# Kernel tuning notes

Measured on AMD Instinct MI355X. Metric: run time of the kernel, lower is better.

## Reference

```python
import jax, jax.numpy as jnp
import numpy as np

V, D, H = 5000, 300, 256
B, T = 16, 512


def setup_inputs() -> dict:
    key = jax.random.key(0)
    ks = jax.random.split(key, 14)
    def w(k, shape):
        return jax.random.normal(k, shape, dtype=jnp.float32) * 0.02
    return {
        "x": jax.random.normal(ks[0], (B, T, V), dtype=jnp.float32),
        "hidden_state": jax.random.normal(ks[1], (1, H), dtype=jnp.float32),
        "context_state": jax.random.normal(ks[2], (1, H), dtype=jnp.float32),
        "E": w(ks[3], (D, V)),      # embedding Linear weight [out,in]
        "Wf": w(ks[4], (H, D)), "Uf": w(ks[5], (H, H)),
        "Wg": w(ks[6], (H, D)), "Ug": w(ks[7], (H, H)),
        "Wi": w(ks[8], (H, D)), "Ui": w(ks[9], (H, H)),
        "Wo": w(ks[10], (H, D)), "Uo": w(ks[11], (H, H)),
        "Wout": w(ks[12], (V, H)),
    }


def reference(x, hidden_state, context_state, E, Wf, Uf, Wg, Ug, Wi, Ui, Wo, Uo, Wout):
    # Precompute all input-side projections in one batched pass: [B,T,D]
    emb = jnp.einsum('btv,dv->btd', x, E)
    # Stack input-gate GEMMs: [B,T,4H]
    Wx = jnp.concatenate([Wf, Wg, Wi, Wo], axis=0)  # [4H, D]
    gates_x = jnp.einsum('btd,gd->btg', emb, Wx)    # [B, T, 4H]
    Uh = jnp.concatenate([Uf, Ug, Ui, Uo], axis=0)  # [4H, H]

    h0 = jnp.broadcast_to(hidden_state, (x.shape[0], hidden_state.shape[-1]))
    c0 = jnp.broadcast_to(context_state, (x.shape[0], context_state.shape[-1]))

    Hn = hidden_state.shape[-1]

    def step(carry, gx):
        h, c = carry
        gh = h @ Uh.T                     # [B, 4H]
        z = gx + gh
        f = jax.nn.sigmoid(z[:, 0*Hn:1*Hn])
        g = jnp.tanh(z[:, 1*Hn:2*Hn])
        i = jax.nn.sigmoid(z[:, 2*Hn:3*Hn])
        o = jax.nn.sigmoid(z[:, 3*Hn:4*Hn])
        c_new = g * i + c * f
        h_new = o * jnp.tanh(c_new)
        # NOTE: faithful to source - output projects g, not h
        out = g @ Wout.T                  # [B, V]
        return (h_new, c_new), out

    _, outs = jax.lax.scan(step, (h0, c0), jnp.swapaxes(gates_x, 0, 1))
    return jnp.swapaxes(outs, 0, 1)       # [B, T, V]
```

## Files before the change

### kernel.cpp

```cpp
#include <hip/hip_runtime.h>
#include <stdint.h>

typedef unsigned short u16;
typedef unsigned int u32;
typedef __attribute__((ext_vector_type(8))) __bf16 bf16x8;
typedef __attribute__((ext_vector_type(4))) float f32x4;
typedef __attribute__((ext_vector_type(4))) u32 u32x4;
typedef __attribute__((ext_vector_type(2))) u32 u32x2;
typedef __attribute__((ext_vector_type(4))) int i32x4;

#define DEV __device__ __forceinline__

constexpr int V = 5000, D = 300, H = 256, BB = 16, T = 512;
constexpr int M = BB * T;
constexpr int DP = 320;
constexpr int KP = 5024;
constexpr int G4 = 1024;
constexpr int NPAD = 5120;

constexpr size_t OFF_EB    = 0;
constexpr size_t OFF_WXB   = OFF_EB    + (size_t)DP * KP * 2;
constexpr size_t OFF_UHB   = OFF_WXB   + (size_t)G4 * DP * 2;
constexpr size_t OFF_WOUTB = OFF_UHB   + (size_t)G4 * H * 2;
constexpr size_t OFF_GATES = OFF_WOUTB + (size_t)NPAD * H * 2;
constexpr size_t OFF_GALL  = OFF_GATES + (size_t)T * BB * G4 * 2;
constexpr size_t OFF_EMB   = OFF_GALL  + (size_t)M * H * 2;

DEV u16 f2bf(float f) {
  u32 i = __builtin_bit_cast(u32, f);
  return (u16)((i + 0x7FFFu + ((i >> 16) & 1u)) >> 16);
}
DEV float bf2f(u16 u) { return __builtin_bit_cast(float, (u32)u << 16); }
DEV f32x4 MFMA(u32x4 a, u32x4 b, f32x4 c) {
  return __builtin_amdgcn_mfma_f32_16x16x32_bf16(
      __builtin_bit_cast(bf16x8, a), __builtin_bit_cast(bf16x8, b), c, 0, 0, 0);
}
DEV i32x4 MFMA8(u32x4 a, u32x4 b, i32x4 c) {
  return __builtin_amdgcn_mfma_i32_16x16x64_i8(
      __builtin_bit_cast(i32x4, a), __builtin_bit_cast(i32x4, b), c, 0, 0, 0);
}
DEV float sigm(float x) { return 1.f / (1.f + __expf(-x)); }
DEV float tanh_s(float x) { float e = __expf(2.f * x); return 1.f - 2.f / (e + 1.f); }

DEV void bar_lds() {
  asm volatile("s_waitcnt lgkmcnt(0)" ::: "memory");
  __builtin_amdgcn_sched_barrier(0);
  __builtin_amdgcn_s_barrier();
  __builtin_amdgcn_sched_barrier(0);
}

__global__ __launch_bounds__(256) void k_prep(
    const float* __restrict__ E, const float* __restrict__ Wf, const float* __restrict__ Wg,
    const float* __restrict__ Wi, const float* __restrict__ Wo,
    const float* __restrict__ Wout, char* __restrict__ ws) {
  u16* Eb = (u16*)(ws + OFF_EB);
  u16* Wxb = (u16*)(ws + OFF_WXB);
  u16* Wob = (u16*)(ws + OFF_WOUTB);

  const int NE = DP * KP, NW = G4 * DP, NWO = NPAD * H;
  const int total = NE + NW + NWO;
  for (int i = blockIdx.x * blockDim.x + threadIdx.x; i < total; i += gridDim.x * blockDim.x) {
    int j = i;
    if (j < NE) {
      int nn = j / KP, k = j % KP;
      Eb[j] = f2bf((nn < D && k < V) ? E[(size_t)nn * V + k] : 0.f);
      continue;
    }
    j -= NE;
    if (j < NW) {
      int r = j / DP, k = j % DP;
      const float* Wp = (r < 256) ? Wf : (r < 512) ? Wg : (r < 768) ? Wi : Wo;
      Wxb[j] = f2bf((k < D) ? Wp[(size_t)(r & 255) * D + k] : 0.f);
      continue;
    }
    j -= NW;
    if (j < NWO) {
      int nn = j / H, k = j % H;
      Wob[j] = f2bf((nn < V) ? Wout[(size_t)nn * H + k] : 0.f);
      continue;
    }
  }
}

__global__ __launch_bounds__(256) void k_prep_u(
    const float* __restrict__ Uf, const float* __restrict__ Ug,
    const float* __restrict__ Ui, const float* __restrict__ Uo, char* __restrict__ ws) {
  char* qU = ws + OFF_UHB;
  float* zsc = (float*)(ws + OFF_UHB + (size_t)G4 * H);
  const int row = blockIdx.x * 4 + (threadIdx.x >> 6);
  const int lane = threadIdx.x & 63;
  const float* Up = (row < 256) ? Uf : (row < 512) ? Ug : (row < 768) ? Ui : Uo;
  f32x4 v = *(const f32x4*)(Up + (size_t)(row & 255) * H + lane * 4);
  float m = fmaxf(fmaxf(fabsf(v[0]), fabsf(v[1])), fmaxf(fabsf(v[2]), fabsf(v[3])));
  for (int i = 1; i < 64; i <<= 1) m = fmaxf(m, __shfl_xor(m, i));
  float inv = (m > 0.f) ? 127.f / m : 0.f;
  int q0 = (int)rintf(v[0] * inv), q1 = (int)rintf(v[1] * inv);
  int q2 = (int)rintf(v[2] * inv), q3 = (int)rintf(v[3] * inv);
  q0 = max(-127, min(127, q0)); q1 = max(-127, min(127, q1));
  q2 = max(-127, min(127, q2)); q3 = max(-127, min(127, q3));
  u32 pk = (u32)(q0 & 255) | ((u32)(q1 & 255) << 8) | ((u32)(q2 & 255) << 16) |
           ((u32)(q3 & 255) << 24);
  *(u32*)(qU + (size_t)row * H + lane * 4) = pk;
  if (lane == 0) zsc[row] = m / 16129.f;
}

__global__ __launch_bounds__(256) void k_emb(const float* __restrict__ x, char* __restrict__ ws) {
  const u16* Eb = (const u16*)(ws + OFF_EB);
  float* emb = (float*)(ws + OFF_EMB);
  __shared__ __align__(16) u16 As[32 * 40];
  __shared__ __align__(16) u16 Bs[320 * 40];

  const int tid = threadIdx.x;
  const int m0 = blockIdx.x * 32;
  const int lane = tid & 63, wv = tid >> 6;
  const int l15 = lane & 15, lc = lane >> 4;
  const int mt = wv & 1, ntb = (wv >> 1) * 10;

  f32x4 acc[10];
#pragma unroll
  for (int j = 0; j < 10; j++) acc[j] = (f32x4){0.f, 0.f, 0.f, 0.f};

  const int ar = tid >> 3, ak = (tid & 7) * 4;

  f32x4 xv0, xv1;
  u32x4 ev0[5], ev1[5];

#define EMB_ISSUE(SFX, KS)                                                        \
  do {                                                                            \
    int k0_ = (KS) * 32;                                                          \
    {                                                                             \
      size_t base_ = (size_t)(m0 + ar) * V + k0_ + ak;                            \
      if (k0_ + ak + 3 < V) {                                                     \
        xv##SFX = *(const f32x4*)(x + base_);                                     \
      } else {                                                                    \
        f32x4 t_;                                                                 \
        t_[0] = (k0_ + ak + 0 < V) ? x[base_ + 0] : 0.f;                          \
        t_[1] = (k0_ + ak + 1 < V) ? x[base_ + 1] : 0.f;                          \
        t_[2] = (k0_ + ak + 2 < V) ? x[base_ + 2] : 0.f;                          \
        t_[3] = (k0_ + ak + 3 < V) ? x[base_ + 3] : 0.f;                          \
        xv##SFX = t_;                                                             \
      }                                                                           \
    }                                                                             \
    _Pragma("unroll") for (int j_ = 0; j_ < 5; j_++) {                            \
      int cc_ = tid + 256 * j_;                                                   \
      int n_ = cc_ >> 2, ko_ = (cc_ & 3) * 8;                                     \
      ev##SFX[j_] = *(const u32x4*)(Eb + (size_t)n_ * KP + k0_ + ko_);            \
    }                                                                             \
  } while (0)

#define EMB_WRITE(SFX)                                                            \
  do {                                                                            \
    union { u16 u[4]; u32x2 v; } ua_;                                             \
    ua_.u[0] = f2bf(xv##SFX[0]); ua_.u[1] = f2bf(xv##SFX[1]);                     \
    ua_.u[2] = f2bf(xv##SFX[2]); ua_.u[3] = f2bf(xv##SFX[3]);                     \
    *(u32x2*)&As[ar * 40 + ak] = ua_.v;                                           \
    _Pragma("unroll") for (int j_ = 0; j_ < 5; j_++) {                            \
      int cc_ = tid + 256 * j_;                                                   \
      int n_ = cc_ >> 2, ko_ = (cc_ & 3) * 8;                                     \
      *(u32x4*)&Bs[n_ * 40 + ko_] = ev##SFX[j_];                                  \
    }                                                                             \
  } while (0)

  auto emb_compute = [&]() {
    u32x4 a = *(const u32x4*)&As[(mt * 16 + l15) * 40 + lc * 8];
#pragma unroll
    for (int j = 0; j < 10; j++) {
      u32x4 b = *(const u32x4*)&Bs[((ntb + j) * 16 + l15) * 40 + lc * 8];
      acc[j] = MFMA(a, b, acc[j]);
    }
  };

  constexpr int NK = 157;
  EMB_ISSUE(0, 0);
  EMB_ISSUE(1, 1);
  for (int ks = 0; ks < NK; ks += 2) {
    __syncthreads();
    EMB_WRITE(0);
    if (ks + 2 < NK) EMB_ISSUE(0, ks + 2);
    __syncthreads();
    emb_compute();
    if (ks + 1 < NK) {
      __syncthreads();
      EMB_WRITE(1);
      if (ks + 3 < NK) EMB_ISSUE(1, ks + 3);
      __syncthreads();
      emb_compute();
    }
  }
#pragma unroll
  for (int j = 0; j < 10; j++) {
    int nn = (ntb + j) * 16 + l15;
    int mrow = m0 + mt * 16 + lc * 4;
#pragma unroll
    for (int r = 0; r < 4; r++) emb[(size_t)(mrow + r) * DP + nn] = acc[j][r];
  }
#undef EMB_ISSUE
#undef EMB_WRITE
}

__global__ __launch_bounds__(256) void k_gates(char* __restrict__ ws) {
  const float* emb = (const float*)(ws + OFF_EMB);
  const u16* Wxb = (const u16*)(ws + OFF_WXB);
  u16* gates = (u16*)(ws + OFF_GATES);
  __shared__ __align__(16) u16 As[64 * 40];
  __shared__ __align__(16) u16 Bs[256 * 40];

  const int tid = threadIdx.x;
  const int blk = blockIdx.x;
  const int m0 = (blk >> 2) * 64, n0 = (blk & 3) * 256;
  const int lane = tid & 63, wv = tid >> 6;
  const int l15 = lane & 15, lc = lane >> 4;

  f32x4 acc[16];
#pragma unroll
  for (int j = 0; j < 16; j++) acc[j] = (f32x4){0.f, 0.f, 0.f, 0.f};

  f32x4 av0[2], av1[2];
  u32x4 bv0[4], bv1[4];

#define GT_ISSUE(SFX, KS)                                                         \
  do {                                                                            \
    int k0_ = (KS) * 32;                                                          \
    _Pragma("unroll") for (int j_ = 0; j_ < 2; j_++) {                            \
      int c_ = tid + 256 * j_;                                                    \
      int r_ = c_ >> 3, ko_ = (c_ & 7) * 4;                                       \
      av##SFX[j_] = *(const f32x4*)(emb + (size_t)(m0 + r_) * DP + k0_ + ko_);    \
    }                                                                             \
    _Pragma("unroll") for (int j_ = 0; j_ < 4; j_++) {                            \
      int c_ = tid + 256 * j_;                                                    \
      int n_ = c_ >> 2, ko_ = (c_ & 3) * 8;                                       \
      bv##SFX[j_] = *(const u32x4*)(Wxb + (size_t)(n0 + n_) * DP + k0_ + ko_);    \
    }                                                                             \
  } while (0)

#define GT_WRITE(SFX)                                                             \
  do {                                                                            \
    _Pragma("unroll") for (int j_ = 0; j_ < 2; j_++) {                            \
      int c_ = tid + 256 * j_;                                                    \
      int r_ = c_ >> 3, ko_ = (c_ & 7) * 4;                                       \
      union { u16 u[4]; u32x2 v; } ua_;                                           \
      ua_.u[0] = f2bf(av##SFX[j_][0]); ua_.u[1] = f2bf(av##SFX[j_][1]);           \
      ua_.u[2] = f2bf(av##SFX[j_][2]); ua_.u[3] = f2bf(av##SFX[j_][3]);           \
      *(u32x2*)&As[r_ * 40 + ko_] = ua_.v;                                        \
    }                                                                             \
    _Pragma("unroll") for (int j_ = 0; j_ < 4; j_++) {                            \
      int c_ = tid + 256 * j_;                                                    \
      int n_ = c_ >> 2, ko_ = (c_ & 3) * 8;                                       \
      *(u32x4*)&Bs[n_ * 40 + ko_] = bv##SFX[j_];                                  \
    }                                                                             \
  } while (0)

  auto gt_compute = [&]() {
    u32x4 a = *(const u32x4*)&As[(wv * 16 + l15) * 40 + lc * 8];
#pragma unroll
    for (int nt = 0; nt < 16; nt++) {
      u32x4 b = *(const u32x4*)&Bs[(nt * 16 + l15) * 40 + lc * 8];
      acc[nt] = MFMA(a, b, acc[nt]);
    }
  };

  constexpr int NK = 10;
  GT_ISSUE(0, 0);
  GT_ISSUE(1, 1);
  for (int ks = 0; ks < NK; ks += 2) {
    __syncthreads();
    GT_WRITE(0);
    if (ks + 2 < NK) GT_ISSUE(0, ks + 2);
    __syncthreads();
    gt_compute();
    __syncthreads();
    GT_WRITE(1);
    if (ks + 3 < NK) GT_ISSUE(1, ks + 3);
    __syncthreads();
    gt_compute();
  }
#pragma unroll
  for (int nt = 0; nt < 16; nt++) {
#pragma unroll
    for (int r = 0; r < 4; r++) {
      int m = m0 + wv * 16 + lc * 4 + r;
      int col = n0 + nt * 16 + l15;
      int q = col >> 8, nn = col & 255;
      gates[(((size_t)(m & (T - 1)) * 16 + (m >> 9)) * 256 + nn) * 4 + q] = f2bf(acc[nt][r]);
    }
  }
#undef GT_ISSUE
#undef GT_WRITE
}

__global__ __launch_bounds__(512) void k_scan(const float* __restrict__ hidden,
                                              const float* __restrict__ ctx,
                                              char* __restrict__ ws) {
  const char* qU = (const char*)(ws + OFF_UHB);
  const float* zsc = (const float*)(ws + OFF_UHB + (size_t)G4 * H);
  const u16* gates = (const u16*)(ws + OFF_GATES);
  u16* gall = (u16*)(ws + OFF_GALL);

  __shared__ __align__(16) char pq[2][2][256];
  __shared__ __align__(16) int zw[2][8][8][2][16];

  const int tid = threadIdx.x;
  const int lane = tid & 63, wv = tid >> 6;
  const int l15 = lane & 15, lc = lane >> 4;

  u32x4 uq[4][2][4];
#pragma unroll
  for (int gg = 0; gg < 4; gg++)
#pragma unroll
    for (int j = 0; j < 2; j++)
#pragma unroll
      for (int kt = 0; kt < 4; kt++)
        uq[gg][j][kt] = *(const u32x4*)(
            qU + (size_t)(gg * 256 + wv * 32 + j * 16 + l15) * H + kt * 64 + lc * 16);

  const int b = lane >> 5, np = lane & 31;
  const int n = wv * 32 + np;
  const int jj = (np >> 4) & 1, rr = np & 15;
  const int b_glob = blockIdx.x * 2 + b;
  float c = ctx[n];
  const float zs0 = zsc[n], zs1 = zsc[n + 256], zs2 = zsc[n + 512], zs3 = zsc[n + 768];
  u32x2 gxc = *(const u32x2*)(gates + (((size_t)0 * 16 + b_glob) * 256 + n) * 4);
  u32x2 gxn = *(const u32x2*)(gates + (((size_t)1 * 16 + b_glob) * 256 + n) * 4);

  {
    const int b0 = tid >> 8, n0i = tid & 255;
    float h0 = hidden[n0i];
    h0 = fminf(3.999f, fmaxf(-3.999f, h0));
    pq[0][b0][n0i] = (char)(int)rintf(h0 * 31.75f);
  }
  __syncthreads();

#pragma unroll 1
  for (int t = 0; t < T; ++t) {
    const int par = t & 1;
    u32x4 bfr[4];
#pragma unroll
    for (int kt = 0; kt < 4; kt++)
      bfr[kt] = *(const u32x4*)&pq[par][l15 & 1][kt * 64 + lc * 16];

    i32x4 acc[4][2];
#pragma unroll
    for (int gg = 0; gg < 4; gg++)
#pragma unroll
      for (int j = 0; j < 2; j++) {
        i32x4 a = {0, 0, 0, 0};
#pragma unroll
        for (int kt = 0; kt < 4; kt++) a = MFMA8(uq[gg][j][kt], bfr[kt], a);
        acc[gg][j] = a;
      }
    if (l15 < 2) {
#pragma unroll
      for (int gg = 0; gg < 4; gg++)
#pragma unroll
        for (int j = 0; j < 2; j++)
          *(i32x4*)&zw[par][wv][gg * 2 + j][l15][lc * 4] = acc[gg][j];
    }
    asm volatile("s_waitcnt lgkmcnt(0)" ::: "memory");
    __builtin_amdgcn_sched_barrier(0);

    const float hs = (t == 0) ? 4.f : 1.f;
    float z0 = (float)zw[par][wv][0 + jj][b][rr] * (zs0 * hs) + bf2f((u16)(gxc[0] & 0xFFFFu));
    float z1 = (float)zw[par][wv][2 + jj][b][rr] * (zs1 * hs) + bf2f((u16)(gxc[0] >> 16));
    float z2 = (float)zw[par][wv][4 + jj][b][rr] * (zs2 * hs) + bf2f((u16)(gxc[1] & 0xFFFFu));
    float z3 = (float)zw[par][wv][6 + jj][b][rr] * (zs3 * hs) + bf2f((u16)(gxc[1] >> 16));
    float fv = sigm(z0), gv = tanh_s(z1), iv = sigm(z2), ov = sigm(z3);
    c = gv * iv + c * fv;
    float hn = ov * tanh_s(c);
    gall[((size_t)b_glob * T + t) * H + n] = f2bf(gv);
    pq[par ^ 1][b][n] = (char)(int)rintf(hn * 127.f);
    gxc = gxn;
    int t2 = (t + 2 < T) ? (t + 2) : t;
    gxn = *(const u32x2*)(gates + (((size_t)t2 * 16 + b_glob) * 256 + n) * 4);
    bar_lds();
  }
}

__global__ __launch_bounds__(256) void k_out(char* __restrict__ ws, float* __restrict__ out) {
  const u16* gall = (const u16*)(ws + OFF_GALL);
  const u16* Wob = (const u16*)(ws + OFF_WOUTB);
  __shared__ __align__(16) u16 As[64 * 40];
  __shared__ __align__(16) u16 Bs[256 * 40];

  const int tid = threadIdx.x;
  const int blk = blockIdx.x;
  const int m0 = (blk / 20) * 64, n0 = (blk % 20) * 256;
  const int lane = tid & 63, wv = tid >> 6;
  const int l15 = lane & 15, lc = lane >> 4;

  f32x4 acc[16];
#pragma unroll
  for (int j = 0; j < 16; j++) acc[j] = (f32x4){0.f, 0.f, 0.f, 0.f};

  u32x4 av0, av1;
  u32x4 bv0[4], bv1[4];

#define OUT_ISSUE(SFX, KS)                                                        \
  do {                                                                            \
    int k0_ = (KS) * 32;                                                          \
    {                                                                             \
      int r_ = tid >> 2, ko_ = (tid & 3) * 8;                                     \
      av##SFX = *(const u32x4*)(gall + (size_t)(m0 + r_) * H + k0_ + ko_);        \
    }                                                                             \
    _Pragma("unroll") for (int j_ = 0; j_ < 4; j_++) {                            \
      int c_ = tid + 256 * j_;                                                    \
      int n_ = c_ >> 2, ko_ = (c_ & 3) * 8;                                       \
      bv##SFX[j_] = *(const u32x4*)(Wob + (size_t)(n0 + n_) * H + k0_ + ko_);     \
    }                                                                             \
  } while (0)

#define OUT_WRITE(SFX)                                                            \
  do {                                                                            \
    {                                                                             \
      int r_ = tid >> 2, ko_ = (tid & 3) * 8;                                     \
      *(u32x4*)&As[r_ * 40 + ko_] = av##SFX;                                      \
    }                                                                             \
    _Pragma("unroll") for (int j_ = 0; j_ < 4; j_++) {                            \
      int c_ = tid + 256 * j_;                                                    \
      int n_ = c_ >> 2, ko_ = (c_ & 3) * 8;                                       \
      *(u32x4*)&Bs[n_ * 40 + ko_] = bv##SFX[j_];                                  \
    }                                                                             \
  } while (0)

  auto out_compute = [&]() {
    u32x4 a = *(const u32x4*)&As[(wv * 16 + l15) * 40 + lc * 8];
#pragma unroll
    for (int nt = 0; nt < 16; nt++) {
      u32x4 b = *(const u32x4*)&Bs[(nt * 16 + l15) * 40 + lc * 8];
      acc[nt] = MFMA(a, b, acc[nt]);
    }
  };

  constexpr int NK = 8;
  OUT_ISSUE(0, 0);
  OUT_ISSUE(1, 1);
  for (int ks = 0; ks < NK; ks += 2) {
    __syncthreads();
    OUT_WRITE(0);
    if (ks + 2 < NK) OUT_ISSUE(0, ks + 2);
    __syncthreads();
    out_compute();
    __syncthreads();
    OUT_WRITE(1);
    if (ks + 3 < NK) OUT_ISSUE(1, ks + 3);
    __syncthreads();
    out_compute();
  }
#pragma unroll
  for (int nt = 0; nt < 16; nt++) {
    int vcol = n0 + nt * 16 + l15;
    if (vcol < V) {
#pragma unroll
      for (int r = 0; r < 4; r++) {
        int m = m0 + wv * 16 + lc * 4 + r;
        out[(size_t)m * V + vcol] = acc[nt][r];
      }
    }
  }
#undef OUT_ISSUE
#undef OUT_WRITE
}

extern "C" void kernel_launch(void* const* d_in, const int* in_sizes, int n_in,
                              void* d_out, int out_size, void* d_ws, size_t ws_size,
                              hipStream_t stream) {
  (void)in_sizes; (void)n_in; (void)out_size; (void)ws_size;
  const float* x      = (const float*)d_in[0];
  const float* hidden = (const float*)d_in[1];
  const float* ctx    = (const float*)d_in[2];
  const float* E      = (const float*)d_in[3];
  const float* Wf     = (const float*)d_in[4];
  const float* Uf     = (const float*)d_in[5];
  const float* Wg     = (const float*)d_in[6];
  const float* Ug     = (const float*)d_in[7];
  const float* Wi     = (const float*)d_in[8];
  const float* Ui     = (const float*)d_in[9];
  const float* Wo     = (const float*)d_in[10];
  const float* Uo     = (const float*)d_in[11];
  const float* Wout   = (const float*)d_in[12];
  char* ws = (char*)d_ws;
  float* out = (float*)d_out;

  hipLaunchKernelGGL(k_prep, dim3(1024), dim3(256), 0, stream,
                     E, Wf, Wg, Wi, Wo, Wout, ws);
  hipLaunchKernelGGL(k_prep_u, dim3(256), dim3(256), 0, stream, Uf, Ug, Ui, Uo, ws);
  hipLaunchKernelGGL(k_emb, dim3(M / 32), dim3(256), 0, stream, x, ws);
  hipLaunchKernelGGL(k_gates, dim3((M / 64) * 4), dim3(256), 0, stream, ws);
  hipLaunchKernelGGL(k_scan, dim3(8), dim3(512), 0, stream, hidden, ctx, ws);
  hipLaunchKernelGGL(k_out, dim3((M / 64) * 20), dim3(256), 0, stream, ws, out);
}
```

Measured before the change: 822.8 us.

## Fuse embedding and gate GEMMs, merge prep kernels, vectorize output stores

Merges the U-quantization prep into the main prep kernel and fuses the embedding GEMM with the gate projection GEMM, keeping the bf16 embedding tile in LDS instead of round-tripping fp32 emb through global memory. The fused kernel uses 512-thread blocks over 256 tiles of 32 rows, reading Wx directly from global in the second stage. The output GEMM now stages accumulators through LDS to emit coalesced 16-byte stores. Risks include lower parallelism (only 256 blocks for the large x-reading GEMM), uncached global reads of Wx, and the tail column guard dropping the last partial vector if V is not a multiple of 4.

```diff
diff --git a/kernel.cpp b/kernel.cpp
--- a/kernel.cpp
+++ b/kernel.cpp
@@ -24,7 +24,6 @@
 constexpr size_t OFF_WOUTB = OFF_UHB   + (size_t)G4 * H * 2;
 constexpr size_t OFF_GATES = OFF_WOUTB + (size_t)NPAD * H * 2;
 constexpr size_t OFF_GALL  = OFF_GATES + (size_t)T * BB * G4 * 2;
-constexpr size_t OFF_EMB   = OFF_GALL  + (size_t)M * H * 2;
 
 DEV u16 f2bf(float f) {
   u32 i = __builtin_bit_cast(u32, f);
@@ -52,14 +51,35 @@
 __global__ __launch_bounds__(256) void k_prep(
     const float* __restrict__ E, const float* __restrict__ Wf, const float* __restrict__ Wg,
     const float* __restrict__ Wi, const float* __restrict__ Wo,
+    const float* __restrict__ Uf, const float* __restrict__ Ug,
+    const float* __restrict__ Ui, const float* __restrict__ Uo,
     const float* __restrict__ Wout, char* __restrict__ ws) {
+  if (blockIdx.x >= 1024) {
+    char* qU = ws + OFF_UHB;
+    float* zsc = (float*)(ws + OFF_UHB + (size_t)G4 * H);
+    const int row = (blockIdx.x - 1024) * 4 + (threadIdx.x >> 6);
+    const int lane = threadIdx.x & 63;
+    const float* Up = (row < 256) ? Uf : (row < 512) ? Ug : (row < 768) ? Ui : Uo;
+    f32x4 v = *(const f32x4*)(Up + (size_t)(row & 255) * H + lane * 4);
+    float m = fmaxf(fmaxf(fabsf(v[0]), fabsf(v[1])), fmaxf(fabsf(v[2]), fabsf(v[3])));
+    for (int i = 1; i < 64; i <<= 1) m = fmaxf(m, __shfl_xor(m, i));
+    float inv = (m > 0.f) ? 127.f / m : 0.f;
+    int q0 = (int)rintf(v[0] * inv), q1 = (int)rintf(v[1] * inv);
+    int q2 = (int)rintf(v[2] * inv), q3 = (int)rintf(v[3] * inv);
+    q0 = max(-127, min(127, q0)); q1 = max(-127, min(127, q1));
+    q2 = max(-127, min(127, q2)); q3 = max(-127, min(127, q3));
+    u32 pk = (u32)(q0 & 255) | ((u32)(q1 & 255) << 8) | ((u32)(q2 & 255) << 16) |
+             ((u32)(q3 & 255) << 24);
+    *(u32*)(qU + (size_t)row * H + lane * 4) = pk;
+    if (lane == 0) zsc[row] = m / 16129.f;
+    return;
+  }
   u16* Eb = (u16*)(ws + OFF_EB);
   u16* Wxb = (u16*)(ws + OFF_WXB);
   u16* Wob = (u16*)(ws + OFF_WOUTB);
-
   const int NE = DP * KP, NW = G4 * DP, NWO = NPAD * H;
   const int total = NE + NW + NWO;
-  for (int i = blockIdx.x * blockDim.x + threadIdx.x; i < total; i += gridDim.x * blockDim.x) {
+  for (int i = blockIdx.x * blockDim.x + threadIdx.x; i < total; i += 1024 * blockDim.x) {
     int j = i;
     if (j < NE) {
       int nn = j / KP, k = j % KP;
@@ -82,54 +102,34 @@
   }
 }
 
-__global__ __launch_bounds__(256) void k_prep_u(
-    const float* __restrict__ Uf, const float* __restrict__ Ug,
-    const float* __restrict__ Ui, const float* __restrict__ Uo, char* __restrict__ ws) {
-  char* qU = ws + OFF_UHB;
-  float* zsc = (float*)(ws + OFF_UHB + (size_t)G4 * H);
-  const int row = blockIdx.x * 4 + (threadIdx.x >> 6);
-  const int lane = threadIdx.x & 63;
-  const float* Up = (row < 256) ? Uf : (row < 512) ? Ug : (row < 768) ? Ui : Uo;
-  f32x4 v = *(const f32x4*)(Up + (size_t)(row & 255) * H + lane * 4);
-  float m = fmaxf(fmaxf(fabsf(v[0]), fabsf(v[1])), fmaxf(fabsf(v[2]), fabsf(v[3])));
-  for (int i = 1; i < 64; i <<= 1) m = fmaxf(m, __shfl_xor(m, i));
-  float inv = (m > 0.f) ? 127.f / m : 0.f;
-  int q0 = (int)rintf(v[0] * inv), q1 = (int)rintf(v[1] * inv);
-  int q2 = (int)rintf(v[2] * inv), q3 = (int)rintf(v[3] * inv);
-  q0 = max(-127, min(127, q0)); q1 = max(-127, min(127, q1));
-  q2 = max(-127, min(127, q2)); q3 = max(-127, min(127, q3));
-  u32 pk = (u32)(q0 & 255) | ((u32)(q1 & 255) << 8) | ((u32)(q2 & 255) << 16) |
-           ((u32)(q3 & 255) << 24);
-  *(u32*)(qU + (size_t)row * H + lane * 4) = pk;
-  if (lane == 0) zsc[row] = m / 16129.f;
-}
-
-__global__ __launch_bounds__(256) void k_emb(const float* __restrict__ x, char* __restrict__ ws) {
-  const u16* Eb = (const u16*)(ws + OFF_EB);
-  float* emb = (float*)(ws + OFF_EMB);
+__global__ __launch_bounds__(512) void k_embgates(const float* __restrict__ x,
+                                                  char* __restrict__ ws) {
   __shared__ __align__(16) u16 As[32 * 40];
   __shared__ __align__(16) u16 Bs[320 * 40];
+  __shared__ __align__(16) u16 embS[32 * 328];
+  const u16* Eb = (const u16*)(ws + OFF_EB);
+  const u16* Wxb = (const u16*)(ws + OFF_WXB);
+  u16* gates = (u16*)(ws + OFF_GATES);
 
   const int tid = threadIdx.x;
-  const int m0 = blockIdx.x * 32;
   const int lane = tid & 63, wv = tid >> 6;
   const int l15 = lane & 15, lc = lane >> 4;
-  const int mt = wv & 1, ntb = (wv >> 1) * 10;
-
-  f32x4 acc[10];
-#pragma unroll
-  for (int j = 0; j < 10; j++) acc[j] = (f32x4){0.f, 0.f, 0.f, 0.f};
-
+  const int it = blockIdx.x;
+  const int tc = it >> 4, b = it & 15;
+  const int m0x = b * T + tc * 32;
+
+  f32x4 acc[5];
+#pragma unroll
+  for (int j = 0; j < 5; j++) acc[j] = (f32x4){0.f, 0.f, 0.f, 0.f};
   const int ar = tid >> 3, ak = (tid & 7) * 4;
-
   f32x4 xv0, xv1;
-  u32x4 ev0[5], ev1[5];
-
-#define EMB_ISSUE(SFX, KS)                                                        \
+  u32x4 ev0[3], ev1[3];
+
+#define WEMB_ISSUE(SFX, KS)                                                       \
   do {                                                                            \
     int k0_ = (KS) * 32;                                                          \
-    {                                                                             \
-      size_t base_ = (size_t)(m0 + ar) * V + k0_ + ak;                            \
+    if (tid < 256) {                                                              \
+      size_t base_ = (size_t)(m0x + ar) * V + k0_ + ak;                           \
       if (k0_ + ak + 3 < V) {                                                     \
         xv##SFX = *(const f32x4*)(x + base_);                                     \
       } else {                                                                    \
@@ -141,151 +141,95 @@
         xv##SFX = t_;                                                             \
       }                                                                           \
     }                                                                             \
-    _Pragma("unroll") for (int j_ = 0; j_ < 5; j_++) {                            \
-      int cc_ = tid + 256 * j_;                                                   \
-      int n_ = cc_ >> 2, ko_ = (cc_ & 3) * 8;                                     \
-      ev##SFX[j_] = *(const u32x4*)(Eb + (size_t)n_ * KP + k0_ + ko_);            \
+    _Pragma("unroll") for (int p_ = 0; p_ < 3; p_++) {                            \
+      int cc_ = tid + 512 * p_;                                                   \
+      if (cc_ < 1280) {                                                           \
+        int n_ = cc_ >> 2, ko_ = (cc_ & 3) * 8;                                   \
+        ev##SFX[p_] = *(const u32x4*)(Eb + (size_t)n_ * KP + k0_ + ko_);          \
+      }                                                                           \
     }                                                                             \
   } while (0)
 
-#define EMB_WRITE(SFX)                                                            \
+#define WEMB_WRITE(SFX)                                                           \
   do {                                                                            \
-    union { u16 u[4]; u32x2 v; } ua_;                                             \
-    ua_.u[0] = f2bf(xv##SFX[0]); ua_.u[1] = f2bf(xv##SFX[1]);                     \
-    ua_.u[2] = f2bf(xv##SFX[2]); ua_.u[3] = f2bf(xv##SFX[3]);                     \
-    *(u32x2*)&As[ar * 40 + ak] = ua_.v;                                           \
-    _Pragma("unroll") for (int j_ = 0; j_ < 5; j_++) {                            \
-      int cc_ = tid + 256 * j_;                                                   \
-      int n_ = cc_ >> 2, ko_ = (cc_ & 3) * 8;                                     \
-      *(u32x4*)&Bs[n_ * 40 + ko_] = ev##SFX[j_];                                  \
+    if (tid < 256) {                                                              \
+      union { u16 u[4]; u32x2 v; } ua_;                                           \
+      ua_.u[0] = f2bf(xv##SFX[0]); ua_.u[1] = f2bf(xv##SFX[1]);                   \
+      ua_.u[2] = f2bf(xv##SFX[2]); ua_.u[3] = f2bf(xv##SFX[3]);                   \
+      *(u32x2*)&As[ar * 40 + ak] = ua_.v;                                         \
+    }                                                                             \
+    _Pragma("unroll") for (int p_ = 0; p_ < 3; p_++) {                            \
+      int cc_ = tid + 512 * p_;                                                   \
+      if (cc_ < 1280) {                                                           \
+        int n_ = cc_ >> 2, ko_ = (cc_ & 3) * 8;                                   \
+        *(u32x4*)&Bs[n_ * 40 + ko_] = ev##SFX[p_];                                \
+      }                                                                           \
     }                                                                             \
   } while (0)
 
-  auto emb_compute = [&]() {
+  const int mt = wv & 1, ntb = (wv >> 1) * 5;
+  auto wemb_compute = [&]() {
     u32x4 a = *(const u32x4*)&As[(mt * 16 + l15) * 40 + lc * 8];
 #pragma unroll
-    for (int j = 0; j < 10; j++) {
-      u32x4 b = *(const u32x4*)&Bs[((ntb + j) * 16 + l15) * 40 + lc * 8];
-      acc[j] = MFMA(a, b, acc[j]);
+    for (int j = 0; j < 5; j++) {
+      u32x4 bb = *(const u32x4*)&Bs[((ntb + j) * 16 + l15) * 40 + lc * 8];
+      acc[j] = MFMA(a, bb, acc[j]);
     }
   };
 
   constexpr int NK = 157;
-  EMB_ISSUE(0, 0);
-  EMB_ISSUE(1, 1);
+  WEMB_ISSUE(0, 0);
+  WEMB_ISSUE(1, 1);
   for (int ks = 0; ks < NK; ks += 2) {
     __syncthreads();
-    EMB_WRITE(0);
-    if (ks + 2 < NK) EMB_ISSUE(0, ks + 2);
-    __syncthreads();
-    emb_compute();
+    WEMB_WRITE(0);
+    if (ks + 2 < NK) WEMB_ISSUE(0, ks + 2);
+    __syncthreads();
+    wemb_compute();
     if (ks + 1 < NK) {
       __syncthreads();
-      EMB_WRITE(1);
-      if (ks + 3 < NK) EMB_ISSUE(1, ks + 3);
+      WEMB_WRITE(1);
+      if (ks + 3 < NK) WEMB_ISSUE(1, ks + 3);
       __syncthreads();
-      emb_compute();
-    }
-  }
-#pragma unroll
-  for (int j = 0; j < 10; j++) {
+      wemb_compute();
+    }
+  }
+#undef WEMB_ISSUE
+#undef WEMB_WRITE
+  __syncthreads();
+#pragma unroll
+  for (int j = 0; j < 5; j++) {
     int nn = (ntb + j) * 16 + l15;
-    int mrow = m0 + mt * 16 + lc * 4;
-#pragma unroll
-    for (int r = 0; r < 4; r++) emb[(size_t)(mrow + r) * DP + nn] = acc[j][r];
-  }
-#undef EMB_ISSUE
-#undef EMB_WRITE
-}
-
-__global__ __launch_bounds__(256) void k_gates(char* __restrict__ ws) {
-  const float* emb = (const float*)(ws + OFF_EMB);
-  const u16* Wxb = (const u16*)(ws + OFF_WXB);
-  u16* gates = (u16*)(ws + OFF_GATES);
-  __shared__ __align__(16) u16 As[64 * 40];
-  __shared__ __align__(16) u16 Bs[256 * 40];
-
-  const int tid = threadIdx.x;
-  const int blk = blockIdx.x;
-  const int m0 = (blk >> 2) * 64, n0 = (blk & 3) * 256;
-  const int lane = tid & 63, wv = tid >> 6;
-  const int l15 = lane & 15, lc = lane >> 4;
-
-  f32x4 acc[16];
-#pragma unroll
-  for (int j = 0; j < 16; j++) acc[j] = (f32x4){0.f, 0.f, 0.f, 0.f};
-
-  f32x4 av0[2], av1[2];
-  u32x4 bv0[4], bv1[4];
-
-#define GT_ISSUE(SFX, KS)                                                         \
-  do {                                                                            \
-    int k0_ = (KS) * 32;                                                          \
-    _Pragma("unroll") for (int j_ = 0; j_ < 2; j_++) {                            \
-      int c_ = tid + 256 * j_;                                                    \
-      int r_ = c_ >> 3, ko_ = (c_ & 7) * 4;                                       \
-      av##SFX[j_] = *(const f32x4*)(emb + (size_t)(m0 + r_) * DP + k0_ + ko_);    \
-    }                                                                             \
-    _Pragma("unroll") for (int j_ = 0; j_ < 4; j_++) {                            \
-      int c_ = tid + 256 * j_;                                                    \
-      int n_ = c_ >> 2, ko_ = (c_ & 3) * 8;                                       \
-      bv##SFX[j_] = *(const u32x4*)(Wxb + (size_t)(n0 + n_) * DP + k0_ + ko_);    \
-    }                                                                             \
-  } while (0)
-
-#define GT_WRITE(SFX)                                                             \
-  do {                                                                            \
-    _Pragma("unroll") for (int j_ = 0; j_ < 2; j_++) {                            \
-      int c_ = tid + 256 * j_;                                                    \
-      int r_ = c_ >> 3, ko_ = (c_ & 7) * 4;                                       \
-      union { u16 u[4]; u32x2 v; } ua_;                                           \
-      ua_.u[0] = f2bf(av##SFX[j_][0]); ua_.u[1] = f2bf(av##SFX[j_][1]);           \
-      ua_.u[2] = f2bf(av##SFX[j_][2]); ua_.u[3] = f2bf(av##SFX[j_][3]);           \
-      *(u32x2*)&As[r_ * 40 + ko_] = ua_.v;                                        \
-    }                                                                             \
-    _Pragma("unroll") for (int j_ = 0; j_ < 4; j_++) {                            \
-      int c_ = tid + 256 * j_;                                                    \
-      int n_ = c_ >> 2, ko_ = (c_ & 3) * 8;                                       \
-      *(u32x4*)&Bs[n_ * 40 + ko_] = bv##SFX[j_];                                  \
-    }                                                                             \
-  } while (0)
-
-  auto gt_compute = [&]() {
-    u32x4 a = *(const u32x4*)&As[(wv * 16 + l15) * 40 + lc * 8];
+#pragma unroll
+    for (int r = 0; r < 4; r++)
+      embS[(mt * 16 + lc * 4 + r) * 328 + nn] = f2bf(acc[j][r]);
+  }
+  __syncthreads();
+
+  const int amt = wv & 1, ngrp = wv >> 1;
+  f32x4 gacc[16];
+#pragma unroll
+  for (int j = 0; j < 16; j++) gacc[j] = (f32x4){0.f, 0.f, 0.f, 0.f};
+#pragma unroll 1
+  for (int kc = 0; kc < 10; kc++) {
+    u32x4 a = *(const u32x4*)&embS[(amt * 16 + l15) * 328 + kc * 32 + lc * 8];
 #pragma unroll
     for (int nt = 0; nt < 16; nt++) {
-      u32x4 b = *(const u32x4*)&Bs[(nt * 16 + l15) * 40 + lc * 8];
-      acc[nt] = MFMA(a, b, acc[nt]);
-    }
-  };
-
-  constexpr int NK = 10;
-  GT_ISSUE(0, 0);
-  GT_ISSUE(1, 1);
-  for (int ks = 0; ks < NK; ks += 2) {
-    __syncthreads();
-    GT_WRITE(0);
-    if (ks + 2 < NK) GT_ISSUE(0, ks + 2);
-    __syncthreads();
-    gt_compute();
-    __syncthreads();
-    GT_WRITE(1);
-    if (ks + 3 < NK) GT_ISSUE(1, ks + 3);
-    __syncthreads();
-    gt_compute();
+      int col = ngrp * 256 + nt * 16 + l15;
+      u32x4 bb = *(const u32x4*)(Wxb + (size_t)col * DP + kc * 32 + lc * 8);
+      gacc[nt] = MFMA(a, bb, gacc[nt]);
+    }
   }
 #pragma unroll
   for (int nt = 0; nt < 16; nt++) {
 #pragma unroll
     for (int r = 0; r < 4; r++) {
-      int m = m0 + wv * 16 + lc * 4 + r;
-      int col = n0 + nt * 16 + l15;
+      int t = tc * 32 + amt * 16 + lc * 4 + r;
+      int col = ngrp * 256 + nt * 16 + l15;
       int q = col >> 8, nn = col & 255;
-      gates[(((size_t)(m & (T - 1)) * 16 + (m >> 9)) * 256 + nn) * 4 + q] = f2bf(acc[nt][r]);
-    }
-  }
-#undef GT_ISSUE
-#undef GT_WRITE
+      gates[(((size_t)t * 16 + b) * 256 + nn) * 4 + q] = f2bf(gacc[nt][r]);
+    }
+  }
 }
 
 __global__ __launch_bounds__(512) void k_scan(const float* __restrict__ hidden,
@@ -380,6 +324,7 @@
   const u16* Wob = (const u16*)(ws + OFF_WOUTB);
   __shared__ __align__(16) u16 As[64 * 40];
   __shared__ __align__(16) u16 Bs[256 * 40];
+  __shared__ __align__(16) float tb[64 * 132];
 
   const int tid = threadIdx.x;
   const int blk = blockIdx.x;
@@ -445,14 +390,25 @@
     __syncthreads();
     out_compute();
   }
-#pragma unroll
-  for (int nt = 0; nt < 16; nt++) {
-    int vcol = n0 + nt * 16 + l15;
-    if (vcol < V) {
-#pragma unroll
-      for (int r = 0; r < 4; r++) {
-        int m = m0 + wv * 16 + lc * 4 + r;
-        out[(size_t)m * V + vcol] = acc[nt][r];
+
+#pragma unroll
+  for (int h = 0; h < 2; h++) {
+    __syncthreads();
+#pragma unroll
+    for (int nt = 0; nt < 8; nt++) {
+#pragma unroll
+      for (int r = 0; r < 4; r++)
+        tb[(wv * 16 + lc * 4 + r) * 132 + nt * 16 + l15] = acc[h * 8 + nt][r];
+    }
+    __syncthreads();
+#pragma unroll
+    for (int cc = 0; cc < 8; cc++) {
+      int idx = cc * 256 + tid;
+      int row = idx >> 5, c4 = (idx & 31) * 4;
+      int gcol = n0 + h * 128 + c4;
+      if (gcol + 3 < V) {
+        f32x4 v = *(const f32x4*)&tb[row * 132 + c4];
+        *(f32x4*)&out[(size_t)(m0 + row) * V + gcol] = v;
       }
     }
   }
@@ -480,11 +436,9 @@
   char* ws = (char*)d_ws;
   float* out = (float*)d_out;
 
-  hipLaunchKernelGGL(k_prep, dim3(1024), dim3(256), 0, stream,
-                     E, Wf, Wg, Wi, Wo, Wout, ws);
-  hipLaunchKernelGGL(k_prep_u, dim3(256), dim3(256), 0, stream, Uf, Ug, Ui, Uo, ws);
-  hipLaunchKernelGGL(k_emb, dim3(M / 32), dim3(256), 0, stream, x, ws);
-  hipLaunchKernelGGL(k_gates, dim3((M / 64) * 4), dim3(256), 0, stream, ws);
+  hipLaunchKernelGGL(k_prep, dim3(1280), dim3(256), 0, stream,
+                     E, Wf, Wg, Wi, Wo, Uf, Ug, Ui, Uo, Wout, ws);
+  hipLaunchKernelGGL(k_embgates, dim3(256), dim3(512), 0, stream, x, ws);
   hipLaunchKernelGGL(k_scan, dim3(8), dim3(512), 0, stream, hidden, ctx, ws);
   hipLaunchKernelGGL(k_out, dim3((M / 64) * 20), dim3(256), 0, stream, ws, out);
 }
```

Result: no change. 822.6 us (-0.0%).
